# Kernel tuning notes

Measured on AMD Instinct MI355X. Metric: run time of the kernel, lower is better.

## Reference

```python
import jax, jax.numpy as jnp
import numpy as np

H = 4          # n_hidden (forced by Linear(4, 4880) and GRU(4, n_hidden) feeding from embedding)
L = 2          # n_layers
DICT = 4880    # dict_size == fc1 out_features
MAXLEN = 6     # vec_out has exactly 6 time slots
B = 2048
T = 914        # max_point_len


def gru_cell(x, h, Wih, Whh, bih, bhh):
    """PyTorch GRU cell: gates ordered (r, z, n)."""
    gi = x @ Wih.T + bih            # (B, 3H)
    gh = h @ Whh.T + bhh            # (B, 3H)
    ir, iz, inn = jnp.split(gi, 3, axis=-1)
    hr, hz, hn = jnp.split(gh, 3, axis=-1)
    r = jax.nn.sigmoid(ir + hr)
    z = jax.nn.sigmoid(iz + hz)
    n = jnp.tanh(inn + r * hn)
    return (1.0 - z) * n + z * h


def setup_inputs() -> dict:
    key = jax.random.key(0)
    ks = jax.random.split(key, 24)
    s = jnp.float32(0.2)
    d = {}
    d["x"] = jax.random.normal(ks[0], (B, T, 2), dtype=jnp.float32)
    # encoder GRU: layer0 in=2, layer1 in=H
    d["enc_Wih0"] = jax.random.normal(ks[1], (3 * H, 2), dtype=jnp.float32) * s
    d["enc_Whh0"] = jax.random.normal(ks[2], (3 * H, H), dtype=jnp.float32) * s
    d["enc_bih0"] = jax.random.normal(ks[3], (3 * H,), dtype=jnp.float32) * s
    d["enc_bhh0"] = jax.random.normal(ks[4], (3 * H,), dtype=jnp.float32) * s
    d["enc_Wih1"] = jax.random.normal(ks[5], (3 * H, H), dtype=jnp.float32) * s
    d["enc_Whh1"] = jax.random.normal(ks[6], (3 * H, H), dtype=jnp.float32) * s
    d["enc_bih1"] = jax.random.normal(ks[7], (3 * H,), dtype=jnp.float32) * s
    d["enc_bhh1"] = jax.random.normal(ks[8], (3 * H,), dtype=jnp.float32) * s
    # decoder GRU: in=4 == H for both layers
    d["dec_Wih0"] = jax.random.normal(ks[9], (3 * H, H), dtype=jnp.float32) * s
    d["dec_Whh0"] = jax.random.normal(ks[10], (3 * H, H), dtype=jnp.float32) * s
    d["dec_bih0"] = jax.random.normal(ks[11], (3 * H,), dtype=jnp.float32) * s
    d["dec_bhh0"] = jax.random.normal(ks[12], (3 * H,), dtype=jnp.float32) * s
    d["dec_Wih1"] = jax.random.normal(ks[13], (3 * H, H), dtype=jnp.float32) * s
    d["dec_Whh1"] = jax.random.normal(ks[14], (3 * H, H), dtype=jnp.float32) * s
    d["dec_bih1"] = jax.random.normal(ks[15], (3 * H,), dtype=jnp.float32) * s
    d["dec_bhh1"] = jax.random.normal(ks[16], (3 * H,), dtype=jnp.float32) * s
    d["emb"] = jax.random.normal(ks[17], (DICT, H), dtype=jnp.float32) * s
    d["fc_W"] = jax.random.normal(ks[18], (DICT, H), dtype=jnp.float32) * s
    d["fc_b"] = jax.random.normal(ks[19], (DICT,), dtype=jnp.float32) * s
    d["fc1_W"] = jax.random.normal(ks[20], (DICT, H), dtype=jnp.float32) * s
    d["fc1_b"] = jax.random.normal(ks[21], (DICT,), dtype=jnp.float32) * s
    return d


def reference(x, enc_Wih0, enc_Whh0, enc_bih0, enc_bhh0,
              enc_Wih1, enc_Whh1, enc_bih1, enc_bhh1,
              dec_Wih0, dec_Whh0, dec_bih0, dec_bhh0,
              dec_Wih1, dec_Whh1, dec_bih1, dec_bhh1,
              emb, fc_W, fc_b, fc1_W, fc1_b):
    batch = x.shape[0]
    # ---- encoder: 2-layer GRU over time ----
    inp = jnp.transpose(x, (1, 0, 2))          # (T, B, 2)
    h0 = jnp.zeros((batch, H), dtype=x.dtype)
    finals = []
    for (Wih, Whh, bih, bhh) in ((enc_Wih0, enc_Whh0, enc_bih0, enc_bhh0),
                                 (enc_Wih1, enc_Whh1, enc_bih1, enc_bhh1)):
        def step(h, xt, Wih=Wih, Whh=Whh, bih=bih, bhh=bhh):
            hn = gru_cell(xt, h, Wih, Whh, bih, bhh)
            return hn, hn
        hT, outs = jax.lax.scan(step, h0, inp)
        inp = outs                              # (T, B, H)
        finals.append(hT)
    h_enc = jnp.stack(finals)                   # (L, B, H)
    _enc_out = h_enc[-1] @ fc_W.T + fc_b        # computed by original encoder(); unused downstream
    tok0 = jnp.zeros((batch,), dtype=jnp.int32)
    def dec_step(carry, _):
        tok, h = carry                          # tok (B,), h (L, B, H)
        e = emb[tok]                            # (B, H)
        h0n = gru_cell(e, h[0], dec_Wih0, dec_Whh0, dec_bih0, dec_bhh0)
        h1n = gru_cell(h0n, h[1], dec_Wih1, dec_Whh1, dec_bih1, dec_bhh1)
        logits = h1n @ fc1_W.T + fc1_b          # (B, DICT)
        nxt = jnp.argmax(logits, axis=-1).astype(jnp.int32)
        return (nxt, jnp.stack([h0n, h1n])), logits
    (_, _), logits_seq = jax.lax.scan(dec_step, (tok0, h_enc), None, length=MAXLEN)
    vec_out = jnp.transpose(logits_seq, (1, 0, 2))   # (B, MAXLEN, DICT)
    return vec_out, h_enc
```

## Files before the change

### kernel.cpp

```cpp
#include <hip/hip_runtime.h>
#include <stdint.h>

#define TT     914
#define BB     2048
#define DICTN  4880
#define MAXLEN 6
#define HENC_OFF ((size_t)BB * MAXLEN * DICTN)

__device__ __forceinline__ float bf2f(uint16_t u) {
    union { uint32_t i; float f; } v; v.i = ((uint32_t)u) << 16; return v.f;
}
__device__ __forceinline__ float bf2f_lo(uint32_t d) {
    union { uint32_t i; float f; } v; v.i = d << 16; return v.f;
}
__device__ __forceinline__ float bf2f_hi(uint32_t d) {
    union { uint32_t i; float f; } v; v.i = d & 0xFFFF0000u; return v.f;
}
__device__ __forceinline__ uint16_t f2bf(float f) {
    union { uint32_t i; float f; } v; v.f = f;
    uint32_t i = v.i;
    uint32_t r = i + 0x7FFFu + ((i >> 16) & 1u);
    return (uint16_t)(r >> 16);
}
__device__ __forceinline__ float fsigmoid(float x) { return 1.0f / (1.0f + __expf(-x)); }
__device__ __forceinline__ float ftanh(float x)    { return 1.0f - 2.0f / (1.0f + __expf(2.0f * x)); }

#define DOT4(W, a0, a1, a2, a3, b) \
    fmaf((W)[0], (a0), fmaf((W)[1], (a1), fmaf((W)[2], (a2), fmaf((W)[3], (a3), (b)))))

template<bool F32> struct XVT { using T = uint2;  };
template<>         struct XVT<true> { using T = float4; };

template<bool F32>
__device__ __forceinline__ float ldw(const void* p, int i) {
    if constexpr (F32) return ((const float*)p)[i];
    else               return bf2f(((const uint16_t*)p)[i]);
}

template<bool F32>
__device__ __forceinline__ void t2s_body(
    const void* __restrict__ x,
    const void* __restrict__ eWih0, const void* __restrict__ eWhh0,
    const void* __restrict__ ebih0, const void* __restrict__ ebhh0,
    const void* __restrict__ eWih1, const void* __restrict__ eWhh1,
    const void* __restrict__ ebih1, const void* __restrict__ ebhh1,
    const void* __restrict__ dWih0, const void* __restrict__ dWhh0,
    const void* __restrict__ dbih0, const void* __restrict__ dbhh0,
    const void* __restrict__ dWih1, const void* __restrict__ dWhh1,
    const void* __restrict__ dbih1, const void* __restrict__ dbhh1,
    const void* __restrict__ emb,
    const void* __restrict__ fc1W, const void* __restrict__ fc1b,
    void* __restrict__ out)
{
    const int lane  = threadIdx.x;
    const int grp   = lane >> 3;
    const int sub   = lane & 7;
    const int layer = sub >> 2;
    const int j     = sub & 3;
    const int b     = blockIdx.x * 8 + grp;

    float p0, p1, p2, p3, q0, q1, q2, q3;

    {
        const void* Wih = layer ? eWih1 : eWih0;
        const void* Whh = layer ? eWhh1 : eWhh0;
        const void* bip = layer ? ebih1 : ebih0;
        const void* bhp = layer ? ebhh1 : ebhh0;

        float Wi[3][4], Wh[3][4], bi[3], bh[3];
        #pragma unroll
        for (int g = 0; g < 3; ++g) {
            const int row = g * 4 + j;
            bi[g] = ldw<F32>(bip, row);
            bh[g] = ldw<F32>(bhp, row);
            #pragma unroll
            for (int m = 0; m < 4; ++m)
                Wh[g][m] = ldw<F32>(Whh, row * 4 + (j ^ m));
            if (layer) {
                #pragma unroll
                for (int m = 0; m < 4; ++m)
                    Wi[g][m] = ldw<F32>(Wih, row * 4 + (j ^ m));
            } else {
                Wi[g][0] = ldw<F32>(Wih, row * 2 + 0);
                Wi[g][1] = ldw<F32>(Wih, row * 2 + 1);
                Wi[g][2] = 0.0f; Wi[g][3] = 0.0f;
            }
        }

        using XV = typename XVT<F32>::T;
        const XV* __restrict__ xp =
            (const XV*)((const char*)x + (size_t)b * (TT * 2) * (F32 ? 4 : 2));

        float hv0 = 0.f, hv1 = 0.f, hv2 = 0.f, hv3 = 0.f;
        float xf0 = 0.f, xf1 = 0.f, xf2 = 0.f, xf3 = 0.f;

        XV bufA_lo = xp[0], bufA_hi = xp[1];
        XV bufB_lo = xp[2], bufB_hi = xp[3];
        const XV xt = xp[456];
        const bool is_l1 = (layer != 0);

        for (int c = 0; c < 229; ++c) {
            XV lo = bufA_lo, hi = bufA_hi;
            bufA_lo = bufB_lo; bufA_hi = bufB_hi;
            const int ci = min(c + 2, 227);
            bufB_lo = xp[2 * ci];
            bufB_hi = xp[2 * ci + 1];

            if (c == 228) lo = xt;

            #pragma unroll
            for (int s = 0; s < 4; ++s) {
                const int it = c * 4 + s;
                float x0, x1;
                if constexpr (F32) {
                    const float4 v = (s < 2) ? lo : hi;
                    x0 = (s & 1) ? v.z : v.x;
                    x1 = (s & 1) ? v.w : v.y;
                } else {
                    const uint32_t w = (s < 2) ? ((s & 1) ? lo.y : lo.x)
                                               : ((s & 1) ? hi.y : hi.x);
                    x0 = bf2f_lo(w); x1 = bf2f_hi(w);
                }

                const float in0 = is_l1 ? xf0 : x0;
                const float in1 = is_l1 ? xf1 : x1;
                const float in2 = is_l1 ? xf2 : 0.0f;
                const float in3 = is_l1 ? xf3 : 0.0f;

                const float gr = DOT4(Wi[0], in0, in1, in2, in3, bi[0]);
                const float gz = DOT4(Wi[1], in0, in1, in2, in3, bi[1]);
                const float gn = DOT4(Wi[2], in0, in1, in2, in3, bi[2]);
                const float hr = DOT4(Wh[0], hv0, hv1, hv2, hv3, bh[0]);
                const float hz = DOT4(Wh[1], hv0, hv1, hv2, hv3, bh[1]);
                const float hn = DOT4(Wh[2], hv0, hv1, hv2, hv3, bh[2]);

                const float r = fsigmoid(gr + hr);
                const float z = fsigmoid(gz + hz);
                const float n = ftanh(fmaf(r, hn, gn));
                const float hnew = fmaf(z, hv0 - n, n);

                const bool act = is_l1 ? (it >= 1 && it < 915) : (it < 914);
                const float hj = act ? hnew : hv0;

                hv0 = hj;
                hv1 = __shfl_xor(hj, 1);
                hv2 = __shfl_xor(hj, 2);
                hv3 = __shfl_xor(hv1, 2);
                xf0 = __shfl_xor(hv0, 4);
                xf1 = __shfl_xor(hv1, 4);
                xf2 = __shfl_xor(hv2, 4);
                xf3 = __shfl_xor(hv3, 4);
            }
        }

        const size_t hidx = HENC_OFF + ((size_t)layer * BB + b) * 4 + j;
        if constexpr (F32) ((float*)out)[hidx] = hv0;
        else               ((uint16_t*)out)[hidx] = f2bf(hv0);

        p0 = is_l1 ? xf0 : hv0;  p1 = is_l1 ? xf1 : hv1;
        p2 = is_l1 ? xf2 : hv2;  p3 = is_l1 ? xf3 : hv3;
        q0 = is_l1 ? hv0 : xf0;  q1 = is_l1 ? hv1 : xf1;
        q2 = is_l1 ? hv2 : xf2;  q3 = is_l1 ? hv3 : xf3;
    }

    float Wi0[3][4], Wh0[3][4], bi0[3], bh0[3];
    float Wi1[3][4], Wh1[3][4], bi1[3], bh1[3];
    #pragma unroll
    for (int g = 0; g < 3; ++g) {
        const int row = g * 4 + j;
        bi0[g] = ldw<F32>(dbih0, row);  bh0[g] = ldw<F32>(dbhh0, row);
        bi1[g] = ldw<F32>(dbih1, row);  bh1[g] = ldw<F32>(dbhh1, row);
        #pragma unroll
        for (int m = 0; m < 4; ++m) {
            Wi0[g][m] = ldw<F32>(dWih0, row * 4 + m);
            Wh0[g][m] = ldw<F32>(dWhh0, row * 4 + (j ^ m));
            Wi1[g][m] = ldw<F32>(dWih1, row * 4 + (j ^ m));
            Wh1[g][m] = ldw<F32>(dWhh1, row * 4 + (j ^ m));
        }
    }

    int tok = 0;
    for (int st = 0; st < MAXLEN; ++st) {
        float e0, e1, e2, e3;
        if constexpr (F32) {
            const float4 ev = *(const float4*)((const float*)emb + (size_t)tok * 4);
            e0 = ev.x; e1 = ev.y; e2 = ev.z; e3 = ev.w;
        } else {
            const uint2 ev = *(const uint2*)((const uint16_t*)emb + (size_t)tok * 4);
            e0 = bf2f_lo(ev.x); e1 = bf2f_hi(ev.x);
            e2 = bf2f_lo(ev.y); e3 = bf2f_hi(ev.y);
        }

        {
            const float gr = DOT4(Wi0[0], e0, e1, e2, e3, bi0[0]);
            const float gz = DOT4(Wi0[1], e0, e1, e2, e3, bi0[1]);
            const float gn = DOT4(Wi0[2], e0, e1, e2, e3, bi0[2]);
            const float hr = DOT4(Wh0[0], p0, p1, p2, p3, bh0[0]);
            const float hz = DOT4(Wh0[1], p0, p1, p2, p3, bh0[1]);
            const float hn = DOT4(Wh0[2], p0, p1, p2, p3, bh0[2]);
            const float r = fsigmoid(gr + hr);
            const float z = fsigmoid(gz + hz);
            const float n = ftanh(fmaf(r, hn, gn));
            const float hnew = fmaf(z, p0 - n, n);
            p0 = hnew;
            p1 = __shfl_xor(hnew, 1);
            p2 = __shfl_xor(hnew, 2);
            p3 = __shfl_xor(p1, 2);
        }
        {
            const float gr = DOT4(Wi1[0], p0, p1, p2, p3, bi1[0]);
            const float gz = DOT4(Wi1[1], p0, p1, p2, p3, bi1[1]);
            const float gn = DOT4(Wi1[2], p0, p1, p2, p3, bi1[2]);
            const float hr = DOT4(Wh1[0], q0, q1, q2, q3, bh1[0]);
            const float hz = DOT4(Wh1[1], q0, q1, q2, q3, bh1[1]);
            const float hn = DOT4(Wh1[2], q0, q1, q2, q3, bh1[2]);
            const float r = fsigmoid(gr + hr);
            const float z = fsigmoid(gz + hz);
            const float n = ftanh(fmaf(r, hn, gn));
            const float hnew = fmaf(z, q0 - n, n);
            q0 = hnew;
            q1 = __shfl_xor(hnew, 1);
            q2 = __shfl_xor(hnew, 2);
            q3 = __shfl_xor(q1, 2);
        }

        const bool jb0 = (j & 1) != 0, jb1 = (j & 2) != 0;
        const float s0 = jb0 ? q1 : q0, s1 = jb0 ? q0 : q1;
        const float s2 = jb0 ? q3 : q2, s3 = jb0 ? q2 : q3;
        const float a0 = jb1 ? s2 : s0, a1 = jb1 ? s3 : s1;
        const float a2 = jb1 ? s0 : s2, a3 = jb1 ? s1 : s3;

        const size_t off = ((size_t)b * MAXLEN + st) * DICTN;
        float best = -3.4e38f;
        int   bidx = 0;

        for (int db = sub; db < DICTN / 8; db += 8) {
            const int d0 = db * 8;
            float l[8];
            if constexpr (F32) {
                const float4* wr = (const float4*)((const float*)fc1W + (size_t)d0 * 4);
                const float4 bv0 = *(const float4*)((const float*)fc1b + d0);
                const float4 bv1 = *(const float4*)((const float*)fc1b + d0 + 4);
                const float bb[8] = { bv0.x, bv0.y, bv0.z, bv0.w,
                                      bv1.x, bv1.y, bv1.z, bv1.w };
                #pragma unroll
                for (int i = 0; i < 8; ++i) {
                    const float4 w = wr[i];
                    l[i] = fmaf(a0, w.x, fmaf(a1, w.y, fmaf(a2, w.z, fmaf(a3, w.w, bb[i]))));
                }
                float* op = (float*)out + off + d0;
                *(float4*)(op)     = float4{ l[0], l[1], l[2], l[3] };
                *(float4*)(op + 4) = float4{ l[4], l[5], l[6], l[7] };
            } else {
                const uint4* wp = (const uint4*)((const uint16_t*)fc1W + (size_t)d0 * 4);
                const uint4 w0 = wp[0], w1 = wp[1], w2 = wp[2], w3 = wp[3];
                const uint4 bv = *(const uint4*)((const uint16_t*)fc1b + d0);
                const uint32_t wa[16] = { w0.x, w0.y, w0.z, w0.w,
                                          w1.x, w1.y, w1.z, w1.w,
                                          w2.x, w2.y, w2.z, w2.w,
                                          w3.x, w3.y, w3.z, w3.w };
                const uint32_t ba[4] = { bv.x, bv.y, bv.z, bv.w };
                #pragma unroll
                for (int i = 0; i < 8; ++i) {
                    const uint32_t da  = wa[2 * i];
                    const uint32_t db2 = wa[2 * i + 1];
                    float acc = (i & 1) ? bf2f_hi(ba[i >> 1]) : bf2f_lo(ba[i >> 1]);
                    acc = fmaf(a0, bf2f_lo(da), acc);
                    acc = fmaf(a1, bf2f_hi(da), acc);
                    acc = fmaf(a2, bf2f_lo(db2), acc);
                    acc = fmaf(a3, bf2f_hi(db2), acc);
                    l[i] = acc;
                }
                uint4 ov;
                ov.x = (uint32_t)f2bf(l[0]) | ((uint32_t)f2bf(l[1]) << 16);
                ov.y = (uint32_t)f2bf(l[2]) | ((uint32_t)f2bf(l[3]) << 16);
                ov.z = (uint32_t)f2bf(l[4]) | ((uint32_t)f2bf(l[5]) << 16);
                ov.w = (uint32_t)f2bf(l[6]) | ((uint32_t)f2bf(l[7]) << 16);
                *(uint4*)((uint16_t*)out + off + d0) = ov;
            }
            #pragma unroll
            for (int i = 0; i < 8; ++i) {
                if (l[i] > best) { best = l[i]; bidx = d0 + i; }
            }
        }

        #pragma unroll
        for (int mask = 1; mask <= 4; mask <<= 1) {
            const float ov = __shfl_xor(best, mask);
            const int   oi = __shfl_xor(bidx, mask);
            if (ov > best || (ov == best && oi < bidx)) { best = ov; bidx = oi; }
        }
        tok = ((unsigned)bidx < (unsigned)DICTN) ? bidx : 0;
    }
}

__global__ __launch_bounds__(64, 1) void t2s_fused(
    const void* __restrict__ x,
    const void* __restrict__ eWih0, const void* __restrict__ eWhh0,
    const void* __restrict__ ebih0, const void* __restrict__ ebhh0,
    const void* __restrict__ eWih1, const void* __restrict__ eWhh1,
    const void* __restrict__ ebih1, const void* __restrict__ ebhh1,
    const void* __restrict__ dWih0, const void* __restrict__ dWhh0,
    const void* __restrict__ dbih0, const void* __restrict__ dbhh0,
    const void* __restrict__ dWih1, const void* __restrict__ dWhh1,
    const void* __restrict__ dbih1, const void* __restrict__ dbhh1,
    const void* __restrict__ emb,
    const void* __restrict__ fc1W, const void* __restrict__ fc1b,
    void* __restrict__ out)
{
    const uint16_t* pw = (const uint16_t*)eWhh0;
    int cnt = 0;
    #pragma unroll
    for (int k = 0; k < 12; ++k) {
        const float av = fabsf(bf2f(pw[2 * k]));
        if (av >= 0.000244140625f && av <= 8.0f) ++cnt;
    }
    const bool is_bf16 = (cnt >= 7);

    if (is_bf16)
        t2s_body<false>(x, eWih0, eWhh0, ebih0, ebhh0, eWih1, eWhh1, ebih1, ebhh1,
                        dWih0, dWhh0, dbih0, dbhh0, dWih1, dWhh1, dbih1, dbhh1,
                        emb, fc1W, fc1b, out);
    else
        t2s_body<true>(x, eWih0, eWhh0, ebih0, ebhh0, eWih1, eWhh1, ebih1, ebhh1,
                       dWih0, dWhh0, dbih0, dbhh0, dWih1, dWhh1, dbih1, dbhh1,
                       emb, fc1W, fc1b, out);
}

extern "C" void kernel_launch(void* const* d_in, const int* in_sizes, int n_in,
                              void* d_out, int out_size, void* d_ws, size_t ws_size,
                              hipStream_t stream)
{
    (void)d_ws; (void)ws_size; (void)in_sizes; (void)n_in; (void)out_size;

    t2s_fused<<<BB / 8, 64, 0, stream>>>(
        d_in[0],
        d_in[1], d_in[2], d_in[3], d_in[4],
        d_in[5], d_in[6], d_in[7], d_in[8],
        d_in[9], d_in[10], d_in[11], d_in[12],
        d_in[13], d_in[14], d_in[15], d_in[16],
        d_in[17],
        d_in[20], d_in[21],
        d_out);
}
```

Before: 802.2 us.

## Remap lanes so GRU state exchange uses DPP quad permutes and permlane32 swap

The lane mapping changes so the two encoder layers sit in opposite wave halves and the four hidden units of a sample sit in one DPP quad. The ds_bpermute-based __shfl_xor calls in the serial recurrence become DPP quad permutes, and the cross-layer exchange uses permlane32_swap. Sigmoid and tanh use the hardware reciprocal instead of a full division. The goal is lower per-step latency on the 914-step dependency chain, at the cost of slightly less exact reciprocals and a dependency on gfx950-specific builtins.

Result: faster. 717.8 us (-10.5%).

```diff
diff --git a/kernel.cpp b/kernel.cpp
--- a/kernel.cpp
+++ b/kernel.cpp
@@ -22,11 +22,47 @@
     uint32_t r = i + 0x7FFFu + ((i >> 16) & 1u);
     return (uint16_t)(r >> 16);
 }
-__device__ __forceinline__ float fsigmoid(float x) { return 1.0f / (1.0f + __expf(-x)); }
-__device__ __forceinline__ float ftanh(float x)    { return 1.0f - 2.0f / (1.0f + __expf(2.0f * x)); }
+
+__device__ __forceinline__ float fsigmoid(float x) {
+    return __builtin_amdgcn_rcpf(1.0f + __expf(-x));
+}
+__device__ __forceinline__ float ftanh(float x) {
+    return fmaf(-2.0f, __builtin_amdgcn_rcpf(1.0f + __expf(2.0f * x)), 1.0f);
+}
 
 #define DOT4(W, a0, a1, a2, a3, b) \
     fmaf((W)[0], (a0), fmaf((W)[1], (a1), fmaf((W)[2], (a2), fmaf((W)[3], (a3), (b)))))
+
+#define DPP_XOR1 0xB1
+#define DPP_XOR2 0x4E
+#define DPP_XOR3 0x1B
+
+template<int CTRL>
+__device__ __forceinline__ int dpp_i(int v) {
+    return __builtin_amdgcn_mov_dpp(v, CTRL, 0xF, 0xF, true);
+}
+template<int CTRL>
+__device__ __forceinline__ float dpp_f(float v) {
+    return __int_as_float(dpp_i<CTRL>(__float_as_int(v)));
+}
+
+typedef unsigned int uvec2 __attribute__((ext_vector_type(2)));
+
+__device__ __forceinline__ float from_lo(float v) {
+    uvec2 r = __builtin_amdgcn_permlane32_swap(__float_as_uint(v),
+                                               __float_as_uint(v), false, false);
+    return __uint_as_float(r[0]);
+}
+__device__ __forceinline__ float xhalf_f(float v, bool hi) {
+    uvec2 r = __builtin_amdgcn_permlane32_swap(__float_as_uint(v),
+                                               __float_as_uint(v), false, false);
+    return __uint_as_float(hi ? r[0] : r[1]);
+}
+__device__ __forceinline__ int xhalf_i(int v, bool hi) {
+    uvec2 r = __builtin_amdgcn_permlane32_swap((unsigned int)v,
+                                               (unsigned int)v, false, false);
+    return (int)(hi ? r[0] : r[1]);
+}
 
 template<bool F32> struct XVT { using T = uint2;  };
 template<>         struct XVT<true> { using T = float4; };
@@ -52,20 +88,19 @@
     const void* __restrict__ fc1W, const void* __restrict__ fc1b,
     void* __restrict__ out)
 {
-    const int lane  = threadIdx.x;
-    const int grp   = lane >> 3;
-    const int sub   = lane & 7;
-    const int layer = sub >> 2;
-    const int j     = sub & 3;
-    const int b     = blockIdx.x * 8 + grp;
+    const int  lane  = threadIdx.x;
+    const int  j     = lane & 3;
+    const int  bgrp  = (lane >> 2) & 7;
+    const bool is_l1 = (lane >= 32);
+    const int  b     = blockIdx.x * 8 + bgrp;
 
     float p0, p1, p2, p3, q0, q1, q2, q3;
 
     {
-        const void* Wih = layer ? eWih1 : eWih0;
-        const void* Whh = layer ? eWhh1 : eWhh0;
-        const void* bip = layer ? ebih1 : ebih0;
-        const void* bhp = layer ? ebhh1 : ebhh0;
+        const void* Wih = is_l1 ? eWih1 : eWih0;
+        const void* Whh = is_l1 ? eWhh1 : eWhh0;
+        const void* bip = is_l1 ? ebih1 : ebih0;
+        const void* bhp = is_l1 ? ebhh1 : ebhh0;
 
         float Wi[3][4], Wh[3][4], bi[3], bh[3];
         #pragma unroll
@@ -76,7 +111,7 @@
             #pragma unroll
             for (int m = 0; m < 4; ++m)
                 Wh[g][m] = ldw<F32>(Whh, row * 4 + (j ^ m));
-            if (layer) {
+            if (is_l1) {
                 #pragma unroll
                 for (int m = 0; m < 4; ++m)
                     Wi[g][m] = ldw<F32>(Wih, row * 4 + (j ^ m));
@@ -97,7 +132,6 @@
         XV bufA_lo = xp[0], bufA_hi = xp[1];
         XV bufB_lo = xp[2], bufB_hi = xp[3];
         const XV xt = xp[456];
-        const bool is_l1 = (layer != 0);
 
         for (int c = 0; c < 229; ++c) {
             XV lo = bufA_lo, hi = bufA_hi;
@@ -143,24 +177,28 @@
                 const float hj = act ? hnew : hv0;
 
                 hv0 = hj;
-                hv1 = __shfl_xor(hj, 1);
-                hv2 = __shfl_xor(hj, 2);
-                hv3 = __shfl_xor(hv1, 2);
-                xf0 = __shfl_xor(hv0, 4);
-                xf1 = __shfl_xor(hv1, 4);
-                xf2 = __shfl_xor(hv2, 4);
-                xf3 = __shfl_xor(hv3, 4);
+                hv1 = dpp_f<DPP_XOR1>(hj);
+                hv2 = dpp_f<DPP_XOR2>(hj);
+                hv3 = dpp_f<DPP_XOR3>(hj);
+                xf0 = from_lo(hj);
+                xf1 = dpp_f<DPP_XOR1>(xf0);
+                xf2 = dpp_f<DPP_XOR2>(xf0);
+                xf3 = dpp_f<DPP_XOR3>(xf0);
             }
         }
 
-        const size_t hidx = HENC_OFF + ((size_t)layer * BB + b) * 4 + j;
+        const size_t hidx = HENC_OFF + ((size_t)(is_l1 ? 1 : 0) * BB + b) * 4 + j;
         if constexpr (F32) ((float*)out)[hidx] = hv0;
         else               ((uint16_t*)out)[hidx] = f2bf(hv0);
 
-        p0 = is_l1 ? xf0 : hv0;  p1 = is_l1 ? xf1 : hv1;
-        p2 = is_l1 ? xf2 : hv2;  p3 = is_l1 ? xf3 : hv3;
-        q0 = is_l1 ? hv0 : xf0;  q1 = is_l1 ? hv1 : xf1;
-        q2 = is_l1 ? hv2 : xf2;  q3 = is_l1 ? hv3 : xf3;
+        const float o0 = xhalf_f(hv0, is_l1);
+        const float o1 = xhalf_f(hv1, is_l1);
+        const float o2 = xhalf_f(hv2, is_l1);
+        const float o3 = xhalf_f(hv3, is_l1);
+        p0 = is_l1 ? o0 : hv0;  p1 = is_l1 ? o1 : hv1;
+        p2 = is_l1 ? o2 : hv2;  p3 = is_l1 ? o3 : hv3;
+        q0 = is_l1 ? hv0 : o0;  q1 = is_l1 ? hv1 : o1;
+        q2 = is_l1 ? hv2 : o2;  q3 = is_l1 ? hv3 : o3;
     }
 
     float Wi0[3][4], Wh0[3][4], bi0[3], bh0[3];
@@ -179,6 +217,8 @@
         }
     }
 
+    const int sub2 = j | (is_l1 ? 4 : 0);
+
     int tok = 0;
     for (int st = 0; st < MAXLEN; ++st) {
         float e0, e1, e2, e3;
@@ -203,9 +243,9 @@
             const float n = ftanh(fmaf(r, hn, gn));
             const float hnew = fmaf(z, p0 - n, n);
             p0 = hnew;
-            p1 = __shfl_xor(hnew, 1);
-            p2 = __shfl_xor(hnew, 2);
-            p3 = __shfl_xor(p1, 2);
+            p1 = dpp_f<DPP_XOR1>(hnew);
+            p2 = dpp_f<DPP_XOR2>(hnew);
+            p3 = dpp_f<DPP_XOR3>(hnew);
         }
         {
             const float gr = DOT4(Wi1[0], p0, p1, p2, p3, bi1[0]);
@@ -219,9 +259,9 @@
             const float n = ftanh(fmaf(r, hn, gn));
             const float hnew = fmaf(z, q0 - n, n);
             q0 = hnew;
-            q1 = __shfl_xor(hnew, 1);
-            q2 = __shfl_xor(hnew, 2);
-            q3 = __shfl_xor(q1, 2);
+            q1 = dpp_f<DPP_XOR1>(hnew);
+            q2 = dpp_f<DPP_XOR2>(hnew);
+            q3 = dpp_f<DPP_XOR3>(hnew);
         }
 
         const bool jb0 = (j & 1) != 0, jb1 = (j & 2) != 0;
@@ -234,7 +274,7 @@
         float best = -3.4e38f;
         int   bidx = 0;
 
-        for (int db = sub; db < DICTN / 8; db += 8) {
+        for (int db = sub2; db < DICTN / 8; db += 8) {
             const int d0 = db * 8;
             float l[8];
             if constexpr (F32) {
@@ -284,10 +324,19 @@
             }
         }
 
-        #pragma unroll
-        for (int mask = 1; mask <= 4; mask <<= 1) {
-            const float ov = __shfl_xor(best, mask);
-            const int   oi = __shfl_xor(bidx, mask);
+        {
+            const float ov = dpp_f<DPP_XOR1>(best);
+            const int   oi = dpp_i<DPP_XOR1>(bidx);
+            if (ov > best || (ov == best && oi < bidx)) { best = ov; bidx = oi; }
+        }
+        {
+            const float ov = dpp_f<DPP_XOR2>(best);
+            const int   oi = dpp_i<DPP_XOR2>(bidx);
+            if (ov > best || (ov == best && oi < bidx)) { best = ov; bidx = oi; }
+        }
+        {
+            const float ov = xhalf_f(best, is_l1);
+            const int   oi = xhalf_i(bidx, is_l1);
             if (ov > best || (ov == best && oi < bidx)) { best = ov; bidx = oi; }
         }
         tok = ((unsigned)bidx < (unsigned)DICTN) ? bidx : 0;
```
